# Kernel tuning notes

Measured on AMD Instinct MI355X. Metric: run time of the kernel, lower is better.

## Reference

```python
import jax, jax.numpy as jnp
import numpy as np

B, L, D, H = 2, 8192, 1024, 16
HD = D // H  # head_dim = 64


def setup_inputs() -> dict:
    key = jax.random.key(0)
    ks = jax.random.split(key, 5)
    s = 1.0 / np.sqrt(D)
    return {
        "x": jax.random.normal(ks[0], (B, L, D), dtype=jnp.float32),
        "Wq": jax.random.normal(ks[1], (D, D), dtype=jnp.float32) * s,
        "bq": jnp.zeros((D,), dtype=jnp.float32),
        "Wk": jax.random.normal(ks[2], (D, D), dtype=jnp.float32) * s,
        "bk": jnp.zeros((D,), dtype=jnp.float32),
        "Wv": jax.random.normal(ks[3], (D, D), dtype=jnp.float32) * s,
        "bv": jnp.zeros((D,), dtype=jnp.float32),
        "Wo": jax.random.normal(ks[4], (D, D), dtype=jnp.float32) * s,
        "bo": jnp.zeros((D,), dtype=jnp.float32),
    }


def _rotary(seq_len, dim):
    pos = jnp.arange(seq_len, dtype=jnp.float32)
    freq = 1.0 / (10000.0 ** (jnp.arange(0, dim, 2, dtype=jnp.float32) / dim))
    ang = pos[:, None] * freq[None, :]               # (L, dim/2)
    sin, cos = jnp.sin(ang), jnp.cos(ang)
    # interleave-duplicate: stack((s,s),-1).reshape(L,dim)  (matches torch code)
    sin = jnp.stack((sin, sin), axis=-1).reshape(seq_len, dim)
    cos = jnp.stack((cos, cos), axis=-1).reshape(seq_len, dim)
    return sin, cos


def _rotate_half(t):
    t1, t2 = jnp.split(t, 2, axis=-1)
    return jnp.concatenate([-t2, t1], axis=-1)


def reference(x, Wq, bq, Wk, bk, Wv, bv, Wo, bo):
    b, l, d = x.shape
    q = (x @ Wq + bq).reshape(b, l, H, HD)
    k = (x @ Wk + bk).reshape(b, l, H, HD)
    v = (x @ Wv + bv).reshape(b, l, H, HD)

    sin, cos = _rotary(l, HD)
    sin = sin[None, :, None, :]  # (1, L, 1, HD)
    cos = cos[None, :, None, :]
    q = q * cos + _rotate_half(q) * sin
    k = k * cos + _rotate_half(k) * sin

    # NOTE: faithful to original — heads NOT transposed to (B,H,L,HD),
    # so scores are (B, L, H, H): attention mixes across heads per position.
    scores = jnp.einsum('blhd,bled->blhe', q, k) / jnp.sqrt(jnp.float32(HD))
    w = jax.nn.softmax(scores, axis=-1)              # dropout = identity (eval)
    out = jnp.einsum('blhe,bled->blhd', w, v).reshape(b, l, d)
    return out @ Wo + bo
```

## Files before the change

kernel.cpp:

```cpp
#include <hip/hip_runtime.h>
#include <hip/hip_bf16.h>

typedef __bf16 bf16_t;
typedef __bf16 bf16x8 __attribute__((ext_vector_type(8)));
typedef float f32x4 __attribute__((ext_vector_type(4)));

#define SEQ_L 8192
#define DMODEL 1024
#define NHEAD 16
#define HDIM 64
static constexpr int MROWS = 2 * SEQ_L;

__device__ __forceinline__ void async_cp16(const bf16_t* g, bf16_t* l) {
  __builtin_amdgcn_global_load_lds(
      (__attribute__((address_space(1))) void*)(void*)(g),
      (__attribute__((address_space(3))) void*)(void*)(l), 16, 0, 0);
}

__global__ __launch_bounds__(256) void f32_to_bf16_k(const float* __restrict__ in,
                                                     bf16_t* __restrict__ out, int n) {
  int i = (blockIdx.x * 256 + threadIdx.x) * 8;
  if (i >= n) return;
  float4 a = *(const float4*)(in + i);
  float4 b = *(const float4*)(in + i + 4);
  bf16x8 o;
  o[0] = (__bf16)a.x; o[1] = (__bf16)a.y; o[2] = (__bf16)a.z; o[3] = (__bf16)a.w;
  o[4] = (__bf16)b.x; o[5] = (__bf16)b.y; o[6] = (__bf16)b.z; o[7] = (__bf16)b.w;
  *(bf16x8*)(out + i) = o;
}

__global__ __launch_bounds__(256) void w_to_bt_k(
    const float* __restrict__ W0, const float* __restrict__ W1,
    const float* __restrict__ W2, const float* __restrict__ W3,
    bf16_t* __restrict__ T0, bf16_t* __restrict__ T1,
    bf16_t* __restrict__ T2, bf16_t* __restrict__ T3) {
  __shared__ float tile[32][33];
  const int z = blockIdx.z;
  const float* W = (z == 0) ? W0 : (z == 1) ? W1 : (z == 2) ? W2 : W3;
  bf16_t* T = (z == 0) ? T0 : (z == 1) ? T1 : (z == 2) ? T2 : T3;
  const int bx = blockIdx.x, by = blockIdx.y;
  const int tx = threadIdx.x, ty = threadIdx.y;
#pragma unroll
  for (int r = 0; r < 4; ++r)
    tile[ty + r * 8][tx] = W[(size_t)(by * 32 + ty + r * 8) * DMODEL + bx * 32 + tx];
  __syncthreads();
#pragma unroll
  for (int r = 0; r < 4; ++r)
    T[(size_t)(bx * 32 + ty + r * 8) * DMODEL + by * 32 + tx] = (bf16_t)tile[tx][ty + r * 8];
}

__global__ __launch_bounds__(256) void rope_tab_k(float2* __restrict__ tab) {
  int i = blockIdx.x * 256 + threadIdx.x;
  int pos = i >> 5, j = i & 31;
  double freq = pow(10000.0, -(double)j / 32.0);
  double ang = (double)pos * freq;
  tab[i] = make_float2((float)cos(ang), (float)sin(ang));
}

template <int MODE>
__global__ __launch_bounds__(256) void gemm_bt(const bf16_t* __restrict__ A,
                                               const bf16_t* __restrict__ Bt,
                                               const float* __restrict__ b0,
                                               const float* __restrict__ b1,
                                               const float* __restrict__ b2,
                                               const float2* __restrict__ rope,
                                               void* __restrict__ O0,
                                               void* __restrict__ O1,
                                               void* __restrict__ O2,
                                               int M, int N, int K) {
  constexpr int BM = 128, BN = 128, BK = 32;
  __shared__ bf16_t As[2][BM * BK];
  __shared__ bf16_t Bs[2][BN * BK];
  const int tid = threadIdx.x;
  const int lane = tid & 63;
  const int wave = tid >> 6;
  const size_t row0 = (size_t)blockIdx.x * BM;
  const int col0 = blockIdx.y * BN;

  const int srow = tid >> 2;
  const int scol = (tid & 3) * 8;
  const bf16_t* gA = A + (row0 + srow) * K + scol;
  const bf16_t* gB = Bt + (size_t)(col0 + srow) * K + scol;

  const int wr = (wave >> 1) * 64;
  const int wc = (wave & 1) * 64;
  const int fr = lane & 15;
  const int fk = (lane >> 4) * 8;

  f32x4 acc[4][4] = {};

  const int nk = K / BK;
  async_cp16(gA, &As[0][tid * 8]);
  async_cp16(gA + 64 * K, &As[0][2048 + tid * 8]);
  async_cp16(gB, &Bs[0][tid * 8]);
  async_cp16(gB + 64 * K, &Bs[0][2048 + tid * 8]);
  __syncthreads();

  int cur = 0;
  for (int kt = 0; kt < nk; ++kt) {
    if (kt + 1 < nk) {
      const bf16_t* a = gA + (kt + 1) * BK;
      const bf16_t* b = gB + (kt + 1) * BK;
      const int nb = cur ^ 1;
      async_cp16(a, &As[nb][tid * 8]);
      async_cp16(a + 64 * K, &As[nb][2048 + tid * 8]);
      async_cp16(b, &Bs[nb][tid * 8]);
      async_cp16(b + 64 * K, &Bs[nb][2048 + tid * 8]);
    }
    bf16x8 af[4], bg[4];
#pragma unroll
    for (int i = 0; i < 4; ++i) {
      af[i] = *(const bf16x8*)(&As[cur][(wr + i * 16 + fr) * BK + fk]);
      bg[i] = *(const bf16x8*)(&Bs[cur][(wc + i * 16 + fr) * BK + fk]);
    }
#pragma unroll
    for (int mi = 0; mi < 4; ++mi)
#pragma unroll
      for (int ni = 0; ni < 4; ++ni)
        acc[mi][ni] = __builtin_amdgcn_mfma_f32_16x16x32_bf16(af[mi], bg[ni], acc[mi][ni], 0, 0, 0);
    __syncthreads();
    cur ^= 1;
  }

  const int which = (MODE == 0) ? (col0 >> 10) : 0;
  const float* bias = (MODE == 0) ? ((which == 0) ? b0 : (which == 1) ? b1 : b2) : b0;
  const int ocol0 = (MODE == 0) ? (col0 - (which << 10)) : col0;
  const bool do_rope = (MODE == 0) && (which < 2);

  const int lr = (lane >> 4) * 4;
  const int lc = lane & 15;
#pragma unroll
  for (int mi = 0; mi < 4; ++mi) {
#pragma unroll
    for (int i = 0; i < 4; ++i) {
      const size_t grow = row0 + wr + mi * 16 + lr + i;
      float vv[4];
#pragma unroll
      for (int ci = 0; ci < 4; ++ci)
        vv[ci] = acc[mi][ci][i] + bias[ocol0 + wc + ci * 16 + lc];
      if (do_rope) {
        const int pos = (int)(grow & (size_t)(SEQ_L - 1));
        const float2* rp = rope + (size_t)pos * 32 + (lc >> 1);
        float rv[4];
#pragma unroll
        for (int ci = 0; ci < 4; ++ci) {
          float2 cs = rp[ci * 8];
          rv[ci] = (ci < 2) ? vv[ci] * cs.x - vv[ci + 2] * cs.y
                            : vv[ci] * cs.x + vv[ci - 2] * cs.y;
        }
#pragma unroll
        for (int ci = 0; ci < 4; ++ci) vv[ci] = rv[ci];
      }
      const size_t cbase = grow * (size_t)DMODEL + ocol0 + wc + lc;
      if constexpr (MODE == 1) {
        float* C = (float*)O0;
#pragma unroll
        for (int ci = 0; ci < 4; ++ci) C[cbase + ci * 16] = vv[ci];
      } else {
        bf16_t* C = (bf16_t*)((which == 0) ? O0 : (which == 1) ? O1 : O2);
#pragma unroll
        for (int ci = 0; ci < 4; ++ci) C[cbase + ci * 16] = (bf16_t)vv[ci];
      }
    }
  }
}

__global__ __launch_bounds__(256) void attn_heads_k(const bf16_t* __restrict__ qb,
                                                    const bf16_t* __restrict__ kb,
                                                    const bf16_t* __restrict__ vb,
                                                    bf16_t* __restrict__ ob) {
  const int t = blockIdx.x * 256 + threadIdx.x;
  const int row = t >> 4;
  const int h = t & 15;
  const size_t rbase = (size_t)row * DMODEL;

  float q[HDIM];
#pragma unroll
  for (int j = 0; j < 8; ++j) {
    bf16x8 v8 = *(const bf16x8*)(qb + rbase + h * HDIM + j * 8);
#pragma unroll
    for (int u = 0; u < 8; ++u) q[j * 8 + u] = (float)v8[u];
  }
  float s[NHEAD];
#pragma unroll
  for (int e = 0; e < NHEAD; ++e) {
    float a = 0.f;
#pragma unroll
    for (int j = 0; j < 8; ++j) {
      bf16x8 k8 = *(const bf16x8*)(kb + rbase + e * HDIM + j * 8);
#pragma unroll
      for (int u = 0; u < 8; ++u) a += q[j * 8 + u] * (float)k8[u];
    }
    s[e] = a * 0.125f;
  }
  float mx = s[0];
#pragma unroll
  for (int e = 1; e < NHEAD; ++e) mx = fmaxf(mx, s[e]);
  float sum = 0.f;
#pragma unroll
  for (int e = 0; e < NHEAD; ++e) {
    s[e] = __expf(s[e] - mx);
    sum += s[e];
  }
  const float inv = 1.f / sum;
  float o[HDIM] = {};
#pragma unroll
  for (int e = 0; e < NHEAD; ++e) {
    const float w = s[e] * inv;
#pragma unroll
    for (int j = 0; j < 8; ++j) {
      bf16x8 v8 = *(const bf16x8*)(vb + rbase + e * HDIM + j * 8);
#pragma unroll
      for (int u = 0; u < 8; ++u) o[j * 8 + u] += w * (float)v8[u];
    }
  }
#pragma unroll
  for (int j = 0; j < 8; ++j) {
    bf16x8 st;
#pragma unroll
    for (int u = 0; u < 8; ++u) st[u] = (__bf16)o[j * 8 + u];
    *(bf16x8*)(ob + rbase + h * HDIM + j * 8) = st;
  }
}

extern "C" void kernel_launch(void* const* d_in, const int* in_sizes, int n_in,
                              void* d_out, int out_size, void* d_ws, size_t ws_size,
                              hipStream_t stream) {
  const float* x = (const float*)d_in[0];
  const float* Wq = (const float*)d_in[1];
  const float* bq = (const float*)d_in[2];
  const float* Wk = (const float*)d_in[3];
  const float* bk = (const float*)d_in[4];
  const float* Wv = (const float*)d_in[5];
  const float* bv = (const float*)d_in[6];
  const float* Wo = (const float*)d_in[7];
  const float* bo = (const float*)d_in[8];

  const int M = MROWS, N = DMODEL, K = DMODEL;

  char* p = (char*)d_ws;
  bf16_t* xb = (bf16_t*)p;    p += (size_t)M * K * 2;
  bf16_t* Wqkvt = (bf16_t*)p; p += (size_t)3 * N * K * 2;
  bf16_t* Wot = (bf16_t*)p;   p += (size_t)N * K * 2;
  bf16_t* qb = (bf16_t*)p;    p += (size_t)M * N * 2;
  bf16_t* kb = (bf16_t*)p;    p += (size_t)M * N * 2;
  bf16_t* vb = (bf16_t*)p;    p += (size_t)M * N * 2;
  bf16_t* ab = (bf16_t*)p;    p += (size_t)M * N * 2;
  float2* rope = (float2*)p;  p += (size_t)SEQ_L * 32 * sizeof(float2);

  bf16_t* Wqt = Wqkvt;
  bf16_t* Wkt = Wqkvt + (size_t)N * K;
  bf16_t* Wvt = Wqkvt + (size_t)2 * N * K;

  f32_to_bf16_k<<<(M * K) / (256 * 8), 256, 0, stream>>>(x, xb, M * K);
  w_to_bt_k<<<dim3(32, 32, 4), dim3(32, 8), 0, stream>>>(Wq, Wk, Wv, Wo, Wqt, Wkt, Wvt, Wot);
  rope_tab_k<<<(SEQ_L * 32) / 256, 256, 0, stream>>>(rope);

  gemm_bt<0><<<dim3(M / 128, (3 * N) / 128), 256, 0, stream>>>(
      xb, Wqkvt, bq, bk, bv, rope, (void*)qb, (void*)kb, (void*)vb, M, 3 * N, K);
  attn_heads_k<<<(M * NHEAD) / 256, 256, 0, stream>>>(qb, kb, vb, ab);
  gemm_bt<1><<<dim3(M / 128, N / 128), 256, 0, stream>>>(
      ab, Wot, bo, nullptr, nullptr, nullptr, d_out, nullptr, nullptr, M, N, K);
}
```

Before: 260.7 us.

## Replace 128x128 GEMM with 256x256 ping-pong swizzled-LDS MFMA kernel

```diff
diff --git a/kernel.cpp b/kernel.cpp
--- a/kernel.cpp
+++ b/kernel.cpp
@@ -16,6 +16,7 @@
       (__attribute__((address_space(1))) void*)(void*)(g),
       (__attribute__((address_space(3))) void*)(void*)(l), 16, 0, 0);
 }
+__device__ __forceinline__ void wg_barrier() { asm volatile("s_barrier" ::: "memory"); }
 
 __global__ __launch_bounds__(256) void f32_to_bf16_k(const float* __restrict__ in,
                                                      bf16_t* __restrict__ out, int n) {
@@ -58,108 +59,189 @@
 }
 
 template <int MODE>
-__global__ __launch_bounds__(256) void gemm_bt(const bf16_t* __restrict__ A,
-                                               const bf16_t* __restrict__ Bt,
-                                               const float* __restrict__ b0,
-                                               const float* __restrict__ b1,
-                                               const float* __restrict__ b2,
-                                               const float2* __restrict__ rope,
-                                               void* __restrict__ O0,
-                                               void* __restrict__ O1,
-                                               void* __restrict__ O2,
-                                               int M, int N, int K) {
-  constexpr int BM = 128, BN = 128, BK = 32;
-  __shared__ bf16_t As[2][BM * BK];
-  __shared__ bf16_t Bs[2][BN * BK];
+__global__ __launch_bounds__(512, 2) void gemm256(
+    const bf16_t* __restrict__ A, const bf16_t* __restrict__ Bt,
+    const float* __restrict__ b0, const float* __restrict__ b1,
+    const float* __restrict__ b2, const float2* __restrict__ rope,
+    void* __restrict__ O0, void* __restrict__ O1, void* __restrict__ O2) {
+  constexpr int K = DMODEL;
+  constexpr int KT = K / 64;
+  __shared__ bf16_t As_[2][256 * 64];
+  __shared__ bf16_t Bs_[2][256 * 64];
   const int tid = threadIdx.x;
   const int lane = tid & 63;
   const int wave = tid >> 6;
-  const size_t row0 = (size_t)blockIdx.x * BM;
-  const int col0 = blockIdx.y * BN;
-
-  const int srow = tid >> 2;
-  const int scol = (tid & 3) * 8;
-  const bf16_t* gA = A + (row0 + srow) * K + scol;
-  const bf16_t* gB = Bt + (size_t)(col0 + srow) * K + scol;
-
-  const int wr = (wave >> 1) * 64;
-  const int wc = (wave & 1) * 64;
+  const int wm = wave >> 2;
+  const int wn = wave & 3;
+  const size_t row0 = (size_t)blockIdx.x * 256;
+  const int col0 = blockIdx.y * 256;
   const int fr = lane & 15;
-  const int fk = (lane >> 4) * 8;
-
-  f32x4 acc[4][4] = {};
-
-  const int nk = K / BK;
-  async_cp16(gA, &As[0][tid * 8]);
-  async_cp16(gA + 64 * K, &As[0][2048 + tid * 8]);
-  async_cp16(gB, &Bs[0][tid * 8]);
-  async_cp16(gB + 64 * K, &Bs[0][2048 + tid * 8]);
-  __syncthreads();
-
-  int cur = 0;
-  for (int kt = 0; kt < nk; ++kt) {
-    if (kt + 1 < nk) {
-      const bf16_t* a = gA + (kt + 1) * BK;
-      const bf16_t* b = gB + (kt + 1) * BK;
-      const int nb = cur ^ 1;
-      async_cp16(a, &As[nb][tid * 8]);
-      async_cp16(a + 64 * K, &As[nb][2048 + tid * 8]);
-      async_cp16(b, &Bs[nb][tid * 8]);
-      async_cp16(b + 64 * K, &Bs[nb][2048 + tid * 8]);
-    }
-    bf16x8 af[4], bg[4];
-#pragma unroll
-    for (int i = 0; i < 4; ++i) {
-      af[i] = *(const bf16x8*)(&As[cur][(wr + i * 16 + fr) * BK + fk]);
-      bg[i] = *(const bf16x8*)(&Bs[cur][(wc + i * 16 + fr) * BK + fk]);
-    }
-#pragma unroll
-    for (int mi = 0; mi < 4; ++mi)
-#pragma unroll
-      for (int ni = 0; ni < 4; ++ni)
-        acc[mi][ni] = __builtin_amdgcn_mfma_f32_16x16x32_bf16(af[mi], bg[ni], acc[mi][ni], 0, 0, 0);
-    __syncthreads();
-    cur ^= 1;
-  }
-
-  const int which = (MODE == 0) ? (col0 >> 10) : 0;
-  const float* bias = (MODE == 0) ? ((which == 0) ? b0 : (which == 1) ? b1 : b2) : b0;
-  const int ocol0 = (MODE == 0) ? (col0 - (which << 10)) : col0;
-  const bool do_rope = (MODE == 0) && (which < 2);
+  const int fkb = (lane >> 4) * 16;
+
+  const int srow = tid >> 3;
+  const int schunk = (tid & 7) ^ ((tid >> 3) & 7);
+  const bf16_t* gA = A + (row0 + srow) * K + schunk * 8;
+  const bf16_t* gB = Bt + ((size_t)col0 + srow) * K + schunk * 8;
+
+#define STAGE_A(j, h)                                  \
+  do {                                                 \
+    const bf16_t* _g = gA + ((h)*128) * K + (j)*64;    \
+    bf16_t* _l = &As_[(j)&1][(h)*8192 + tid * 8];      \
+    async_cp16(_g, _l);                                \
+    async_cp16(_g + 64 * K, _l + 4096);                \
+  } while (0)
+#define STAGE_B(j, h)                                  \
+  do {                                                 \
+    const bf16_t* _g = gB + ((h)*128) * K + (j)*64;    \
+    bf16_t* _l = &Bs_[(j)&1][(h)*8192 + tid * 8];      \
+    async_cp16(_g, _l);                                \
+    async_cp16(_g + 64 * K, _l + 4096);                \
+  } while (0)
+#define RD(base, row, kh)                                                    \
+  (*(const bf16x8*)((const char*)(base) +                                    \
+                    (((row)*128 + ((kh)*64 + fkb)) ^ (((row)&7) << 4))))
+
+  f32x4 acc[8][4] = {};
+  bf16x8 af[4][2], bf0[2][2], bf1[2][2];
+
+  STAGE_A(0, 0); STAGE_A(0, 1);
+  STAGE_B(0, 0); STAGE_B(0, 1);
+  STAGE_B(1, 0); STAGE_B(1, 1);
+  asm volatile("s_waitcnt vmcnt(4)" ::: "memory");
+  wg_barrier();
+
+  for (int m = 0; m < KT; ++m) {
+    const bf16_t* Ac = &As_[m & 1][0];
+    const bf16_t* Bc = &Bs_[m & 1][0];
+#pragma unroll
+    for (int f = 0; f < 4; ++f) {
+      const int r = wm * 128 + f * 16 + fr;
+      af[f][0] = RD(Ac, r, 0);
+      af[f][1] = RD(Ac, r, 1);
+    }
+#pragma unroll
+    for (int f = 0; f < 2; ++f) {
+      const int r = wn * 64 + f * 16 + fr;
+      bf0[f][0] = RD(Bc, r, 0);
+      bf0[f][1] = RD(Bc, r, 1);
+    }
+    if (m + 1 < KT) STAGE_A(m + 1, 0);
+    wg_barrier();
+    __builtin_amdgcn_s_setprio(1);
+#pragma unroll
+    for (int f = 0; f < 4; ++f)
+#pragma unroll
+      for (int n = 0; n < 2; ++n)
+#pragma unroll
+        for (int kh = 0; kh < 2; ++kh)
+          acc[f][n] = __builtin_amdgcn_mfma_f32_16x16x32_bf16(af[f][kh], bf0[n][kh], acc[f][n], 0, 0, 0);
+    __builtin_amdgcn_s_setprio(0);
+    wg_barrier();
+#pragma unroll
+    for (int f = 0; f < 2; ++f) {
+      const int r = wn * 64 + (2 + f) * 16 + fr;
+      bf1[f][0] = RD(Bc, r, 0);
+      bf1[f][1] = RD(Bc, r, 1);
+    }
+    if (m + 1 < KT) STAGE_A(m + 1, 1);
+    wg_barrier();
+    __builtin_amdgcn_s_setprio(1);
+#pragma unroll
+    for (int f = 0; f < 4; ++f)
+#pragma unroll
+      for (int n = 0; n < 2; ++n)
+#pragma unroll
+        for (int kh = 0; kh < 2; ++kh)
+          acc[f][2 + n] = __builtin_amdgcn_mfma_f32_16x16x32_bf16(af[f][kh], bf1[n][kh], acc[f][2 + n], 0, 0, 0);
+    __builtin_amdgcn_s_setprio(0);
+    wg_barrier();
+#pragma unroll
+    for (int f = 0; f < 4; ++f) {
+      const int r = wm * 128 + (4 + f) * 16 + fr;
+      af[f][0] = RD(Ac, r, 0);
+      af[f][1] = RD(Ac, r, 1);
+    }
+    if (m + 2 < KT) STAGE_B(m + 2, 0);
+    wg_barrier();
+    __builtin_amdgcn_s_setprio(1);
+#pragma unroll
+    for (int f = 0; f < 4; ++f)
+#pragma unroll
+      for (int n = 0; n < 2; ++n)
+#pragma unroll
+        for (int kh = 0; kh < 2; ++kh)
+          acc[4 + f][2 + n] = __builtin_amdgcn_mfma_f32_16x16x32_bf16(af[f][kh], bf1[n][kh], acc[4 + f][2 + n], 0, 0, 0);
+    __builtin_amdgcn_s_setprio(0);
+    wg_barrier();
+    if (m + 2 < KT) {
+      STAGE_B(m + 2, 1);
+      asm volatile("s_waitcnt vmcnt(4)" ::: "memory");
+    } else if (m + 1 < KT) {
+      asm volatile("s_waitcnt vmcnt(0)" ::: "memory");
+    }
+    wg_barrier();
+    __builtin_amdgcn_s_setprio(1);
+#pragma unroll
+    for (int f = 0; f < 4; ++f)
+#pragma unroll
+      for (int n = 0; n < 2; ++n)
+#pragma unroll
+        for (int kh = 0; kh < 2; ++kh)
+          acc[4 + f][n] = __builtin_amdgcn_mfma_f32_16x16x32_bf16(af[f][kh], bf0[n][kh], acc[4 + f][n], 0, 0, 0);
+    __builtin_amdgcn_s_setprio(0);
+    wg_barrier();
+  }
+#undef STAGE_A
+#undef STAGE_B
+#undef RD
 
   const int lr = (lane >> 4) * 4;
   const int lc = lane & 15;
-#pragma unroll
-  for (int mi = 0; mi < 4; ++mi) {
+  const int gcol = col0 + wn * 64;
+  int which = 0;
+  const float* bias = b0;
+  int ocol = gcol;
+  if constexpr (MODE == 0) {
+    which = gcol >> 10;
+    bias = (which == 0) ? b0 : (which == 1) ? b1 : b2;
+    ocol = gcol - (which << 10);
+  }
+  const bool do_rope = (MODE == 0) && (which < 2);
+  bf16_t* Cb = nullptr;
+  float* Cf = nullptr;
+  if constexpr (MODE == 0)
+    Cb = (bf16_t*)((which == 0) ? O0 : (which == 1) ? O1 : O2);
+  else
+    Cf = (float*)O0;
+
+#pragma unroll
+  for (int mf = 0; mf < 8; ++mf) {
 #pragma unroll
     for (int i = 0; i < 4; ++i) {
-      const size_t grow = row0 + wr + mi * 16 + lr + i;
+      const size_t grow = row0 + wm * 128 + mf * 16 + lr + i;
       float vv[4];
 #pragma unroll
-      for (int ci = 0; ci < 4; ++ci)
-        vv[ci] = acc[mi][ci][i] + bias[ocol0 + wc + ci * 16 + lc];
+      for (int n = 0; n < 4; ++n) vv[n] = acc[mf][n][i] + bias[ocol + n * 16 + lc];
       if (do_rope) {
         const int pos = (int)(grow & (size_t)(SEQ_L - 1));
         const float2* rp = rope + (size_t)pos * 32 + (lc >> 1);
         float rv[4];
 #pragma unroll
-        for (int ci = 0; ci < 4; ++ci) {
-          float2 cs = rp[ci * 8];
-          rv[ci] = (ci < 2) ? vv[ci] * cs.x - vv[ci + 2] * cs.y
-                            : vv[ci] * cs.x + vv[ci - 2] * cs.y;
+        for (int n = 0; n < 4; ++n) {
+          float2 cs = rp[n * 8];
+          rv[n] = (n < 2) ? vv[n] * cs.x - vv[n + 2] * cs.y
+                          : vv[n] * cs.x + vv[n - 2] * cs.y;
         }
 #pragma unroll
-        for (int ci = 0; ci < 4; ++ci) vv[ci] = rv[ci];
+        for (int n = 0; n < 4; ++n) vv[n] = rv[n];
       }
-      const size_t cbase = grow * (size_t)DMODEL + ocol0 + wc + lc;
+      const size_t cbase = grow * (size_t)DMODEL + ocol + lc;
       if constexpr (MODE == 1) {
-        float* C = (float*)O0;
-#pragma unroll
-        for (int ci = 0; ci < 4; ++ci) C[cbase + ci * 16] = vv[ci];
+#pragma unroll
+        for (int n = 0; n < 4; ++n) Cf[cbase + n * 16] = vv[n];
       } else {
-        bf16_t* C = (bf16_t*)((which == 0) ? O0 : (which == 1) ? O1 : O2);
-#pragma unroll
-        for (int ci = 0; ci < 4; ++ci) C[cbase + ci * 16] = (bf16_t)vv[ci];
+#pragma unroll
+        for (int n = 0; n < 4; ++n) Cb[cbase + n * 16] = (bf16_t)vv[n];
       }
     }
   }
@@ -256,9 +338,9 @@
   w_to_bt_k<<<dim3(32, 32, 4), dim3(32, 8), 0, stream>>>(Wq, Wk, Wv, Wo, Wqt, Wkt, Wvt, Wot);
   rope_tab_k<<<(SEQ_L * 32) / 256, 256, 0, stream>>>(rope);
 
-  gemm_bt<0><<<dim3(M / 128, (3 * N) / 128), 256, 0, stream>>>(
-      xb, Wqkvt, bq, bk, bv, rope, (void*)qb, (void*)kb, (void*)vb, M, 3 * N, K);
+  gemm256<0><<<dim3(M / 256, (3 * N) / 256), 512, 0, stream>>>(
+      xb, Wqkvt, bq, bk, bv, rope, (void*)qb, (void*)kb, (void*)vb);
   attn_heads_k<<<(M * NHEAD) / 256, 256, 0, stream>>>(qb, kb, vb, ab);
-  gemm_bt<1><<<dim3(M / 128, N / 128), 256, 0, stream>>>(
-      ab, Wot, bo, nullptr, nullptr, nullptr, d_out, nullptr, nullptr, M, N, K);
-}
+  gemm256<1><<<dim3(M / 256, N / 256), 512, 0, stream>>>(
+      ab, Wot, bo, nullptr, nullptr, nullptr, d_out, nullptr, nullptr);
+}
```

Result: faster. 242.3 us (-7.1%).
